# Performance work log

Hardware: AMD Instinct MI355X
Metric: run time of the kernel (lower is better)

Reference implementation:

```python
import jax, jax.numpy as jnp
import numpy as np

EMBED = 1024
HEADS = 16
HEAD_DIM = EMBED // HEADS


def setup_inputs() -> dict:
    key = jax.random.key(0)
    k_x, k_q, k_k, k_v, k_o, k_b = jax.random.split(key, 6)
    s = 1.0 / np.sqrt(EMBED)
    return {
        "x": jax.random.normal(k_x, (4, 2048, EMBED), dtype=jnp.float32),
        "Wq": jax.random.uniform(k_q, (EMBED, EMBED), jnp.float32, -s, s),
        "Wk": jax.random.uniform(k_k, (EMBED, EMBED), jnp.float32, -s, s),
        "Wv": jax.random.uniform(k_v, (EMBED, EMBED), jnp.float32, -s, s),
        "Wo": jax.random.uniform(k_o, (EMBED, EMBED), jnp.float32, -s, s),
        "bo": jax.random.uniform(k_b, (EMBED,), jnp.float32, -s, s),
    }


def reference(x, Wq, Wk, Wv, Wo, bo):
    B, S, E = x.shape
    H, D = HEADS, HEAD_DIM
    # torch nn.Linear: y = x @ W.T
    q = (x @ Wq.T).reshape(B, S, H, D).transpose(0, 2, 1, 3)  # [B,H,S,D]
    k = (x @ Wk.T).reshape(B, S, H, D).transpose(0, 2, 1, 3)
    v = (x @ Wv.T).reshape(B, S, H, D).transpose(0, 2, 1, 3)
    # NOTE: module scales by sqrt(embed_size), not sqrt(head_dim)
    scores = jnp.einsum("bhqd,bhkd->bhqk", q, k) / jnp.sqrt(jnp.float32(E))
    causal = jnp.triu(jnp.ones((S, S), dtype=bool), k=1)
    scores = jnp.where(causal, -jnp.inf, scores)
    attn = jax.nn.softmax(scores, axis=-1)
    out = jnp.einsum("bhqk,bhkd->bhqd", attn, v)  # [B,H,S,D]
    out = out.transpose(0, 2, 1, 3).reshape(B, S, E)
    return out @ Wo.T + bo
```

## Files before the change

### kernel.cpp

```cpp
#include <hip/hip_runtime.h>


#define E_DIM 1024
#define S_LEN 2048
#define BATCH 4
#define NHEAD 16
#define HDIM  64

using short8 = __attribute__((ext_vector_type(8))) short;
using f32x4  = __attribute__((ext_vector_type(4))) float;
using f32x16 = __attribute__((ext_vector_type(16))) float;
using i32x4  = __attribute__((ext_vector_type(4))) int;

#define GLD16(gp, lp) __builtin_amdgcn_global_load_lds( \
    (const __attribute__((address_space(1))) void*)(gp), \
    (__attribute__((address_space(3))) void*)(lp), 16, 0, 0)

__device__ inline unsigned short f2bf(float f) {
    unsigned int u = __builtin_bit_cast(unsigned int, f);
    u += 0x7FFFu + ((u >> 16) & 1u);
    return (unsigned short)(u >> 16);
}

__device__ inline unsigned int cvt_pk_bf16(float a, float b) {
    unsigned int r;
    asm("v_cvt_pk_bf16_f32 %0, %1, %2" : "=v"(r) : "v"(a), "v"(b));
    return r;
}

__global__ __launch_bounds__(256) void cvt_all(
        const float* __restrict__ x,  const float* __restrict__ wq,
        const float* __restrict__ wk, const float* __restrict__ wv,
        const float* __restrict__ wo,
        unsigned short* __restrict__ xb, unsigned short* __restrict__ wb) {
    const int bid = blockIdx.x;
    const float* src;
    unsigned short* dst;
    int blk;
    if (bid < 8192) { src = x; dst = xb; blk = bid; }
    else {
        const int wsel = (bid - 8192) >> 10;
        blk = (bid - 8192) & 1023;
        src = (wsel == 0) ? wq : (wsel == 1) ? wk : (wsel == 2) ? wv : wo;
        dst = wb + (size_t)wsel * 1048576;
    }
    const int i = (blk * 256 + threadIdx.x) * 4;
    float4 v = *reinterpret_cast<const float4*>(src + i);
    ushort4 o;
    o.x = f2bf(v.x); o.y = f2bf(v.y); o.z = f2bf(v.z); o.w = f2bf(v.w);
    *reinterpret_cast<ushort4*>(dst + i) = o;
}

__global__ __launch_bounds__(256) void gemm_qkv(
        const unsigned short* __restrict__ xb,
        const unsigned short* __restrict__ wb,
        unsigned short* __restrict__ qkv) {
    const int z = blockIdx.z;
    const unsigned short* Bw = wb + (size_t)z * (E_DIM * E_DIM);
    unsigned short* Out = qkv + (size_t)z * ((size_t)BATCH * NHEAD * S_LEN * HDIM);
    const int m0 = blockIdx.x * 128, n0 = blockIdx.y * 128;
    const int tid = threadIdx.x;
    const int lane = tid & 63, w = tid >> 6;
    const int wm = w >> 1, wn = w & 1;
    const int col = lane & 15, hi = lane >> 4;

    __shared__ __align__(16) unsigned short Alds[128 * 32];
    __shared__ __align__(16) unsigned short Blds[128 * 32];

    const int srow = tid >> 2;
    const int sc8  = (tid & 3) * 8;
    const int wofs = w * 512;

    f32x4 acc[4][4] = {};

    for (int kt = 0; kt < E_DIM / 32; ++kt) {
        const int k0 = kt * 32;
        GLD16(xb + (size_t)(m0 + srow) * E_DIM + k0 + sc8,       &Alds[wofs]);
        GLD16(xb + (size_t)(m0 + 64 + srow) * E_DIM + k0 + sc8,  &Alds[2048 + wofs]);
        GLD16(Bw + (size_t)(n0 + srow) * E_DIM + k0 + sc8,       &Blds[wofs]);
        GLD16(Bw + (size_t)(n0 + 64 + srow) * E_DIM + k0 + sc8,  &Blds[2048 + wofs]);
        __syncthreads();
        short8 af[4], bf[4];
#pragma unroll
        for (int mt = 0; mt < 4; ++mt)
            af[mt] = *reinterpret_cast<const short8*>(&Alds[(wm * 64 + mt * 16 + col) * 32 + hi * 8]);
#pragma unroll
        for (int nt = 0; nt < 4; ++nt)
            bf[nt] = *reinterpret_cast<const short8*>(&Blds[(wn * 64 + nt * 16 + col) * 32 + hi * 8]);
#pragma unroll
        for (int mt = 0; mt < 4; ++mt)
#pragma unroll
            for (int nt = 0; nt < 4; ++nt)
                acc[mt][nt] = __builtin_amdgcn_mfma_f32_16x16x32_bf16(af[mt], bf[nt], acc[mt][nt], 0, 0, 0);
        __syncthreads();
    }

    const float scale = (z == 0) ? (0.03125f * 1.44269504f) : 1.0f;
#pragma unroll
    for (int mt = 0; mt < 4; ++mt) {
#pragma unroll
        for (int nt = 0; nt < 4; ++nt) {
#pragma unroll
            for (int b = 0; b < 4; ++b) {
                int m = m0 + wm * 64 + mt * 16 + hi * 4 + b;
                int n = n0 + wn * 64 + nt * 16 + col;
                int bidx = m >> 11, s = m & 2047;
                int h = n >> 6, d = n & 63;
                size_t off = (((size_t)(bidx * NHEAD + h)) * S_LEN + s) * HDIM + d;
                Out[off] = f2bf(acc[mt][nt][b] * scale);
            }
        }
    }
}

__global__ __launch_bounds__(256, 4) void attn_fwd(
        const unsigned short* __restrict__ Q,
        const unsigned short* __restrict__ K,
        const unsigned short* __restrict__ V,
        unsigned short* __restrict__ Out) {
    const int g = blockIdx.x;
    const int qt = 15 - (g >> 6);
    const int bh = (g & 7) + ((g >> 3) & 7) * 8;
    const int b_idx = bh >> 4, h = bh & 15;
    const int tid = threadIdx.x, lane = tid & 63, w = tid >> 6;
    const int l31 = lane & 31, b5 = lane >> 5;
    const bool lo32 = (b5 == 0);
    const int rsw = (l31 & 7) << 3;

    const unsigned short* Qb = Q + (size_t)bh * (S_LEN * HDIM);
    const unsigned short* Kb = K + (size_t)bh * (S_LEN * HDIM);
    const unsigned short* Vb = V + (size_t)bh * (S_LEN * HDIM);

    __shared__ __align__(16) unsigned short Klds[64 * 64];
    __shared__ __align__(16) unsigned short Vt[64 * 64];

    const int kr = tid >> 3, kc8 = (tid & 7) * 8;
    const int ksw = kc8 ^ ((kr & 7) << 3);
    const int vr = tid & 63, vc8 = (tid >> 6) * 8;

    const int nt = 2 * qt + 2;
    const int q0w = qt * 128 + w * 32;
    const int qg = q0w + l31;

    short8 qf[4];
    {
        const unsigned short* qrow = Qb + (size_t)qg * HDIM;
#pragma unroll
        for (int dc = 0; dc < 4; ++dc)
            qf[dc] = *reinterpret_cast<const short8*>(qrow + dc * 16 + b5 * 8);
    }

    f32x16 ot0 = {}, ot1 = {};
    float mrun = -INFINITY, lsum = 0.f;

    short8 pk0 = *reinterpret_cast<const short8*>(Kb + (size_t)kr * HDIM + kc8);
    short8 pk1 = *reinterpret_cast<const short8*>(Kb + (size_t)(32 + kr) * HDIM + kc8);
    short8 pv0 = *reinterpret_cast<const short8*>(Vb + (size_t)vr * HDIM + vc8);
    short8 pv1 = *reinterpret_cast<const short8*>(Vb + (size_t)vr * HDIM + vc8 + 32);

    for (int t = 0; t < nt; ++t) {
        const int kv0 = t * 64;
        __syncthreads();
        *reinterpret_cast<short8*>(&Klds[kr * 64 + ksw]) = pk0;
        *reinterpret_cast<short8*>(&Klds[(kr + 32) * 64 + ksw]) = pk1;
#pragma unroll
        for (int j = 0; j < 8; ++j) {
            const int d0 = vc8 + j;
            const int vsw = vr ^ ((d0 & 7) << 3);
            Vt[d0 * 64 + vsw]        = (unsigned short)pv0[j];
            Vt[(d0 + 32) * 64 + vsw] = (unsigned short)pv1[j];
        }
        if (t < nt - 1) {
            const int kn = kv0 + 64;
            pk0 = *reinterpret_cast<const short8*>(Kb + (size_t)(kn + kr) * HDIM + kc8);
            pk1 = *reinterpret_cast<const short8*>(Kb + (size_t)(kn + 32 + kr) * HDIM + kc8);
            pv0 = *reinterpret_cast<const short8*>(Vb + (size_t)(kn + vr) * HDIM + vc8);
            pv1 = *reinterpret_cast<const short8*>(Vb + (size_t)(kn + vr) * HDIM + vc8 + 32);
        }
        __syncthreads();

        if (kv0 <= q0w + 31) {
            f32x16 st0 = {}, st1 = {};
            __builtin_amdgcn_s_setprio(1);
#pragma unroll
            for (int dc = 0; dc < 4; ++dc) {
                const int co = dc * 16 + b5 * 8;
                short8 kfA = *reinterpret_cast<const short8*>(&Klds[l31 * 64 + (co ^ rsw)]);
                short8 kfB = *reinterpret_cast<const short8*>(&Klds[(32 + l31) * 64 + (co ^ rsw)]);
                st0 = __builtin_amdgcn_mfma_f32_32x32x16_bf16(kfA, qf[dc], st0, 0, 0, 0);
                st1 = __builtin_amdgcn_mfma_f32_32x32x16_bf16(kfB, qf[dc], st1, 0, 0, 0);
            }
            __builtin_amdgcn_s_setprio(0);

            if (kv0 + 63 > q0w) {
#pragma unroll
                for (int r = 0; r < 16; ++r) {
                    const int krow = (r & 3) + 8 * (r >> 2) + 4 * b5;
                    if (kv0 + krow > qg)      st0[r] = -INFINITY;
                    if (kv0 + 32 + krow > qg) st1[r] = -INFINITY;
                }
            }

            float vm = st0[0];
#pragma unroll
            for (int r = 1; r < 16; ++r) vm = fmaxf(vm, st0[r]);
#pragma unroll
            for (int r = 0; r < 16; ++r) vm = fmaxf(vm, st1[r]);
            vm = fmaxf(vm, __shfl_xor(vm, 32));
            if (__any(vm > mrun + 11.5f)) {
                const float mnew = fmaxf(mrun, vm);
                const float fac = exp2f(mrun - mnew);
                mrun = mnew;
                lsum *= fac;
#pragma unroll
                for (int r = 0; r < 16; ++r) { ot0[r] *= fac; ot1[r] *= fac; }
            }

#pragma unroll
            for (int kc = 0; kc < 4; ++kc) {
                const int r0 = (kc & 1) * 8;
                float pe[8];
#pragma unroll
                for (int i = 0; i < 8; ++i) {
                    const float sv = (kc < 2) ? st0[r0 + i] : st1[r0 + i];
                    pe[i] = exp2f(sv - mrun);
                    lsum += pe[i];
                }
                const unsigned int W0 = cvt_pk_bf16(pe[0], pe[1]);
                const unsigned int W1 = cvt_pk_bf16(pe[2], pe[3]);
                const unsigned int W2 = cvt_pk_bf16(pe[4], pe[5]);
                const unsigned int W3 = cvt_pk_bf16(pe[6], pe[7]);
                const unsigned int t0 = (unsigned int)__shfl_xor((int)W0, 32);
                const unsigned int t1 = (unsigned int)__shfl_xor((int)W1, 32);
                const unsigned int t2 = (unsigned int)__shfl_xor((int)W2, 32);
                const unsigned int t3 = (unsigned int)__shfl_xor((int)W3, 32);
                i32x4 wv;
                wv[0] = (int)(lo32 ? W0 : t2);
                wv[1] = (int)(lo32 ? W1 : t3);
                wv[2] = (int)(lo32 ? t0 : W2);
                wv[3] = (int)(lo32 ? t1 : W3);
                const short8 pf = __builtin_bit_cast(short8, wv);

                const int co = kc * 16 + b5 * 8;
                short8 vf0 = *reinterpret_cast<const short8*>(&Vt[l31 * 64 + (co ^ rsw)]);
                short8 vf1 = *reinterpret_cast<const short8*>(&Vt[(32 + l31) * 64 + (co ^ rsw)]);
                __builtin_amdgcn_s_setprio(1);
                ot0 = __builtin_amdgcn_mfma_f32_32x32x16_bf16(vf0, pf, ot0, 0, 0, 0);
                ot1 = __builtin_amdgcn_mfma_f32_32x32x16_bf16(vf1, pf, ot1, 0, 0, 0);
                __builtin_amdgcn_s_setprio(0);
            }
        }
    }

    const float lfull = lsum + __shfl_xor(lsum, 32);
    const float inv = 1.0f / lfull;
    const size_t base = ((size_t)(b_idx * S_LEN + qg)) * E_DIM + h * HDIM;
#pragma unroll
    for (int r2 = 0; r2 < 8; ++r2) {
        const int d0 = 2 * (r2 & 1) + 8 * (r2 >> 1) + 4 * b5;
        const unsigned int u0 = cvt_pk_bf16(ot0[2 * r2] * inv, ot0[2 * r2 + 1] * inv);
        const unsigned int u1 = cvt_pk_bf16(ot1[2 * r2] * inv, ot1[2 * r2 + 1] * inv);
        *reinterpret_cast<unsigned int*>(const_cast<unsigned short*>(Out) + base + d0) = u0;
        *reinterpret_cast<unsigned int*>(const_cast<unsigned short*>(Out) + base + 32 + d0) = u1;
    }
}

__global__ __launch_bounds__(256) void gemm_out(
        const unsigned short* __restrict__ Ab,
        const unsigned short* __restrict__ Bw,
        const float* __restrict__ bias,
        float* __restrict__ Out) {
    const int m0 = blockIdx.x * 128, n0 = blockIdx.y * 128;
    const int tid = threadIdx.x;
    const int lane = tid & 63, w = tid >> 6;
    const int wm = w >> 1, wn = w & 1;
    const int col = lane & 15, hi = lane >> 4;

    __shared__ __align__(16) unsigned short Alds[128 * 32];
    __shared__ __align__(16) unsigned short Blds[128 * 32];

    const int srow = tid >> 2;
    const int sc8  = (tid & 3) * 8;
    const int wofs = w * 512;

    f32x4 acc[4][4] = {};

    for (int kt = 0; kt < E_DIM / 32; ++kt) {
        const int k0 = kt * 32;
        GLD16(Ab + (size_t)(m0 + srow) * E_DIM + k0 + sc8,       &Alds[wofs]);
        GLD16(Ab + (size_t)(m0 + 64 + srow) * E_DIM + k0 + sc8,  &Alds[2048 + wofs]);
        GLD16(Bw + (size_t)(n0 + srow) * E_DIM + k0 + sc8,       &Blds[wofs]);
        GLD16(Bw + (size_t)(n0 + 64 + srow) * E_DIM + k0 + sc8,  &Blds[2048 + wofs]);
        __syncthreads();
        short8 af[4], bf[4];
#pragma unroll
        for (int mt = 0; mt < 4; ++mt)
            af[mt] = *reinterpret_cast<const short8*>(&Alds[(wm * 64 + mt * 16 + col) * 32 + hi * 8]);
#pragma unroll
        for (int nt = 0; nt < 4; ++nt)
            bf[nt] = *reinterpret_cast<const short8*>(&Blds[(wn * 64 + nt * 16 + col) * 32 + hi * 8]);
#pragma unroll
        for (int mt = 0; mt < 4; ++mt)
#pragma unroll
            for (int nt = 0; nt < 4; ++nt)
                acc[mt][nt] = __builtin_amdgcn_mfma_f32_16x16x32_bf16(af[mt], bf[nt], acc[mt][nt], 0, 0, 0);
        __syncthreads();
    }

#pragma unroll
    for (int mt = 0; mt < 4; ++mt) {
#pragma unroll
        for (int nt = 0; nt < 4; ++nt) {
#pragma unroll
            for (int b = 0; b < 4; ++b) {
                int m = m0 + wm * 64 + mt * 16 + hi * 4 + b;
                int n = n0 + wn * 64 + nt * 16 + col;
                Out[(size_t)m * E_DIM + n] = acc[mt][nt][b] + bias[n];
            }
        }
    }
}

extern "C" void kernel_launch(void* const* d_in, const int* in_sizes, int n_in,
                              void* d_out, int out_size, void* d_ws, size_t ws_size,
                              hipStream_t stream) {
    const float* x  = (const float*)d_in[0];
    const float* Wq = (const float*)d_in[1];
    const float* Wk = (const float*)d_in[2];
    const float* Wv = (const float*)d_in[3];
    const float* Wo = (const float*)d_in[4];
    const float* bo = (const float*)d_in[5];
    float* out = (float*)d_out;

    unsigned short* ws   = (unsigned short*)d_ws;
    unsigned short* xb   = ws;
    unsigned short* wb   = xb + (size_t)8192 * 1024;
    unsigned short* qkv  = wb + (size_t)4 * 1024 * 1024;
    unsigned short* attn = qkv + (size_t)3 * 8192 * 1024;

    cvt_all<<<12288, 256, 0, stream>>>(x, Wq, Wk, Wv, Wo, xb, wb);
    gemm_qkv<<<dim3(64, 8, 3), 256, 0, stream>>>(xb, wb, qkv);
    attn_fwd<<<1024, 256, 0, stream>>>(qkv, qkv + 8388608, qkv + 2 * 8388608, attn);
    gemm_out<<<dim3(64, 8), 256, 0, stream>>>(attn, wb + 3 * 1048576, bo, out);
}
```

Baseline: 196.2 us.

## Load K fragments directly into registers and double-buffer V in LDS

Drops the shared-memory K tile. Each wave now loads its K MFMA fragments straight from global memory into registers, prefetching the next tile right after the QK^T MFMAs. V gets a double-buffered LDS tile so one of the two per-iteration barriers can go, and the row-max reduction becomes a tree. This removes LDS write/read traffic and a barrier for K, at the cost of four times more global (L2) K reads per block and higher register pressure under the 256x4 launch bound.

Result: slower. 274.2 us (+39.7%).

```diff
diff --git a/kernel.cpp b/kernel.cpp
--- a/kernel.cpp
+++ b/kernel.cpp
@@ -131,11 +131,8 @@
     const unsigned short* Kb = K + (size_t)bh * (S_LEN * HDIM);
     const unsigned short* Vb = V + (size_t)bh * (S_LEN * HDIM);
 
-    __shared__ __align__(16) unsigned short Klds[64 * 64];
-    __shared__ __align__(16) unsigned short Vt[64 * 64];
-
-    const int kr = tid >> 3, kc8 = (tid & 7) * 8;
-    const int ksw = kc8 ^ ((kr & 7) << 3);
+    __shared__ __align__(16) unsigned short Vt[2][64 * 64];
+
     const int vr = tid & 63, vc8 = (tid >> 6) * 8;
 
     const int nt = 2 * qt + 2;
@@ -153,27 +150,30 @@
     f32x16 ot0 = {}, ot1 = {};
     float mrun = -INFINITY, lsum = 0.f;
 
-    short8 pk0 = *reinterpret_cast<const short8*>(Kb + (size_t)kr * HDIM + kc8);
-    short8 pk1 = *reinterpret_cast<const short8*>(Kb + (size_t)(32 + kr) * HDIM + kc8);
     short8 pv0 = *reinterpret_cast<const short8*>(Vb + (size_t)vr * HDIM + vc8);
     short8 pv1 = *reinterpret_cast<const short8*>(Vb + (size_t)vr * HDIM + vc8 + 32);
+    short8 kf0[4], kf1[4];
+    {
+        const size_t ro = (size_t)l31 * HDIM + b5 * 8;
+#pragma unroll
+        for (int dc = 0; dc < 4; ++dc) {
+            kf0[dc] = *reinterpret_cast<const short8*>(Kb + ro + dc * 16);
+            kf1[dc] = *reinterpret_cast<const short8*>(Kb + ro + 32 * HDIM + dc * 16);
+        }
+    }
 
     for (int t = 0; t < nt; ++t) {
         const int kv0 = t * 64;
-        __syncthreads();
-        *reinterpret_cast<short8*>(&Klds[kr * 64 + ksw]) = pk0;
-        *reinterpret_cast<short8*>(&Klds[(kr + 32) * 64 + ksw]) = pk1;
+        unsigned short* Vw = &Vt[t & 1][0];
 #pragma unroll
         for (int j = 0; j < 8; ++j) {
             const int d0 = vc8 + j;
             const int vsw = vr ^ ((d0 & 7) << 3);
-            Vt[d0 * 64 + vsw]        = (unsigned short)pv0[j];
-            Vt[(d0 + 32) * 64 + vsw] = (unsigned short)pv1[j];
+            Vw[d0 * 64 + vsw]        = (unsigned short)pv0[j];
+            Vw[(d0 + 32) * 64 + vsw] = (unsigned short)pv1[j];
         }
         if (t < nt - 1) {
             const int kn = kv0 + 64;
-            pk0 = *reinterpret_cast<const short8*>(Kb + (size_t)(kn + kr) * HDIM + kc8);
-            pk1 = *reinterpret_cast<const short8*>(Kb + (size_t)(kn + 32 + kr) * HDIM + kc8);
             pv0 = *reinterpret_cast<const short8*>(Vb + (size_t)(kn + vr) * HDIM + vc8);
             pv1 = *reinterpret_cast<const short8*>(Vb + (size_t)(kn + vr) * HDIM + vc8 + 32);
         }
@@ -184,13 +184,19 @@
             __builtin_amdgcn_s_setprio(1);
 #pragma unroll
             for (int dc = 0; dc < 4; ++dc) {
-                const int co = dc * 16 + b5 * 8;
-                short8 kfA = *reinterpret_cast<const short8*>(&Klds[l31 * 64 + (co ^ rsw)]);
-                short8 kfB = *reinterpret_cast<const short8*>(&Klds[(32 + l31) * 64 + (co ^ rsw)]);
-                st0 = __builtin_amdgcn_mfma_f32_32x32x16_bf16(kfA, qf[dc], st0, 0, 0, 0);
-                st1 = __builtin_amdgcn_mfma_f32_32x32x16_bf16(kfB, qf[dc], st1, 0, 0, 0);
+                st0 = __builtin_amdgcn_mfma_f32_32x32x16_bf16(kf0[dc], qf[dc], st0, 0, 0, 0);
+                st1 = __builtin_amdgcn_mfma_f32_32x32x16_bf16(kf1[dc], qf[dc], st1, 0, 0, 0);
             }
             __builtin_amdgcn_s_setprio(0);
+
+            if (t < nt - 1) {
+                const size_t ro = (size_t)(kv0 + 64 + l31) * HDIM + b5 * 8;
+#pragma unroll
+                for (int dc = 0; dc < 4; ++dc) {
+                    kf0[dc] = *reinterpret_cast<const short8*>(Kb + ro + dc * 16);
+                    kf1[dc] = *reinterpret_cast<const short8*>(Kb + ro + 32 * HDIM + dc * 16);
+                }
+            }
 
             if (kv0 + 63 > q0w) {
 #pragma unroll
@@ -201,11 +207,14 @@
                 }
             }
 
-            float vm = st0[0];
-#pragma unroll
-            for (int r = 1; r < 16; ++r) vm = fmaxf(vm, st0[r]);
-#pragma unroll
-            for (int r = 0; r < 16; ++r) vm = fmaxf(vm, st1[r]);
+            float tm[16];
+#pragma unroll
+            for (int r = 0; r < 16; ++r) tm[r] = fmaxf(st0[r], st1[r]);
+#pragma unroll
+            for (int r = 0; r < 8; ++r) tm[r] = fmaxf(tm[r], tm[r + 8]);
+#pragma unroll
+            for (int r = 0; r < 4; ++r) tm[r] = fmaxf(tm[r], tm[r + 4]);
+            float vm = fmaxf(fmaxf(tm[0], tm[1]), fmaxf(tm[2], tm[3]));
             vm = fmaxf(vm, __shfl_xor(vm, 32));
             if (__any(vm > mrun + 11.5f)) {
                 const float mnew = fmaxf(mrun, vm);
@@ -242,8 +251,9 @@
                 const short8 pf = __builtin_bit_cast(short8, wv);
 
                 const int co = kc * 16 + b5 * 8;
-                short8 vf0 = *reinterpret_cast<const short8*>(&Vt[l31 * 64 + (co ^ rsw)]);
-                short8 vf1 = *reinterpret_cast<const short8*>(&Vt[(32 + l31) * 64 + (co ^ rsw)]);
+                const unsigned short* Vc = &Vt[t & 1][0];
+                short8 vf0 = *reinterpret_cast<const short8*>(&Vc[l31 * 64 + (co ^ rsw)]);
+                short8 vf1 = *reinterpret_cast<const short8*>(&Vc[(32 + l31) * 64 + (co ^ rsw)]);
                 __builtin_amdgcn_s_setprio(1);
                 ot0 = __builtin_amdgcn_mfma_f32_32x32x16_bf16(vf0, pf, ot0, 0, 0, 0);
                 ot1 = __builtin_amdgcn_mfma_f32_32x32x16_bf16(vf1, pf, ot1, 0, 0, 0);
```

## Use 256-row query and key tiles with 512-thread blocks and async K loads

Applied to the files above, without the earlier changes.

The attention kernel now uses 512-thread blocks covering 256 query rows and stages 256 keys per iteration, with four 64-key sub-steps of compute per stage. K is copied straight into LDS with global_load_lds instead of passing through registers, and the row-max reduction becomes a tree. Larger tiles mean fewer barriers and more reuse of each K/V tile per block. The cost is four times the LDS per block, lower occupancy, coarser causal granularity that leaves more threads idle, and only 512 blocks in the grid.

Measured after the change: 178.3 us. 9.1% less time.

```diff
diff --git a/kernel.cpp b/kernel.cpp
--- a/kernel.cpp
+++ b/kernel.cpp
@@ -113,13 +113,13 @@
     }
 }
 
-__global__ __launch_bounds__(256, 4) void attn_fwd(
+__global__ __launch_bounds__(512, 2) void attn_fwd(
         const unsigned short* __restrict__ Q,
         const unsigned short* __restrict__ K,
         const unsigned short* __restrict__ V,
         unsigned short* __restrict__ Out) {
     const int g = blockIdx.x;
-    const int qt = 15 - (g >> 6);
+    const int qt = 7 - (g >> 6);
     const int bh = (g & 7) + ((g >> 3) & 7) * 8;
     const int b_idx = bh >> 4, h = bh & 15;
     const int tid = threadIdx.x, lane = tid & 63, w = tid >> 6;
@@ -131,15 +131,15 @@
     const unsigned short* Kb = K + (size_t)bh * (S_LEN * HDIM);
     const unsigned short* Vb = V + (size_t)bh * (S_LEN * HDIM);
 
-    __shared__ __align__(16) unsigned short Klds[64 * 64];
-    __shared__ __align__(16) unsigned short Vt[64 * 64];
-
-    const int kr = tid >> 3, kc8 = (tid & 7) * 8;
-    const int ksw = kc8 ^ ((kr & 7) << 3);
+    __shared__ __align__(16) unsigned short Klds[256 * 64];
+    __shared__ __align__(16) unsigned short Vt[64 * 256];
+
+    const int krl  = lane >> 3;
+    const int kcsw = ((lane & 7) * 8) ^ (krl << 3);
     const int vr = tid & 63, vc8 = (tid >> 6) * 8;
 
-    const int nt = 2 * qt + 2;
-    const int q0w = qt * 128 + w * 32;
+    const int nt = qt + 1;
+    const int q0w = qt * 256 + w * 32;
     const int qg = q0w + l31;
 
     short8 qf[4];
@@ -153,59 +153,80 @@
     f32x16 ot0 = {}, ot1 = {};
     float mrun = -INFINITY, lsum = 0.f;
 
-    short8 pk0 = *reinterpret_cast<const short8*>(Kb + (size_t)kr * HDIM + kc8);
-    short8 pk1 = *reinterpret_cast<const short8*>(Kb + (size_t)(32 + kr) * HDIM + kc8);
-    short8 pv0 = *reinterpret_cast<const short8*>(Vb + (size_t)vr * HDIM + vc8);
-    short8 pv1 = *reinterpret_cast<const short8*>(Vb + (size_t)vr * HDIM + vc8 + 32);
+    short8 pv0 = *reinterpret_cast<const short8*>(Vb + (size_t)(vr) * HDIM + vc8);
+    short8 pv1 = *reinterpret_cast<const short8*>(Vb + (size_t)(64 + vr) * HDIM + vc8);
+    short8 pv2 = *reinterpret_cast<const short8*>(Vb + (size_t)(128 + vr) * HDIM + vc8);
+    short8 pv3 = *reinterpret_cast<const short8*>(Vb + (size_t)(192 + vr) * HDIM + vc8);
 
     for (int t = 0; t < nt; ++t) {
-        const int kv0 = t * 64;
-        __syncthreads();
-        *reinterpret_cast<short8*>(&Klds[kr * 64 + ksw]) = pk0;
-        *reinterpret_cast<short8*>(&Klds[(kr + 32) * 64 + ksw]) = pk1;
+        const int kv0 = t * 256;
+        __syncthreads();
+#pragma unroll
+        for (int i = 0; i < 4; ++i) {
+            const int rowbase = 8 * (8 * i + w);
+            GLD16(Kb + (size_t)(kv0 + rowbase + krl) * HDIM + kcsw,
+                  &Klds[rowbase * 64]);
+        }
 #pragma unroll
         for (int j = 0; j < 8; ++j) {
             const int d0 = vc8 + j;
-            const int vsw = vr ^ ((d0 & 7) << 3);
-            Vt[d0 * 64 + vsw]        = (unsigned short)pv0[j];
-            Vt[(d0 + 32) * 64 + vsw] = (unsigned short)pv1[j];
+            const int sj = (d0 & 7) << 3;
+            Vt[d0 * 256 + ((vr)       ^ sj)] = (unsigned short)pv0[j];
+            Vt[d0 * 256 + ((64 + vr)  ^ sj)] = (unsigned short)pv1[j];
+            Vt[d0 * 256 + ((128 + vr) ^ sj)] = (unsigned short)pv2[j];
+            Vt[d0 * 256 + ((192 + vr) ^ sj)] = (unsigned short)pv3[j];
         }
         if (t < nt - 1) {
-            const int kn = kv0 + 64;
-            pk0 = *reinterpret_cast<const short8*>(Kb + (size_t)(kn + kr) * HDIM + kc8);
-            pk1 = *reinterpret_cast<const short8*>(Kb + (size_t)(kn + 32 + kr) * HDIM + kc8);
+            const int kn = kv0 + 256;
             pv0 = *reinterpret_cast<const short8*>(Vb + (size_t)(kn + vr) * HDIM + vc8);
-            pv1 = *reinterpret_cast<const short8*>(Vb + (size_t)(kn + vr) * HDIM + vc8 + 32);
-        }
-        __syncthreads();
-
-        if (kv0 <= q0w + 31) {
+            pv1 = *reinterpret_cast<const short8*>(Vb + (size_t)(kn + 64 + vr) * HDIM + vc8);
+            pv2 = *reinterpret_cast<const short8*>(Vb + (size_t)(kn + 128 + vr) * HDIM + vc8);
+            pv3 = *reinterpret_cast<const short8*>(Vb + (size_t)(kn + 192 + vr) * HDIM + vc8);
+        }
+        __syncthreads();
+
+#pragma unroll
+        for (int s4 = 0; s4 < 4; ++s4) {
+            const int kvs = kv0 + 64 * s4;
+            if (kvs > q0w + 31) break;
+            const int ksb = 64 * s4;
+
             f32x16 st0 = {}, st1 = {};
             __builtin_amdgcn_s_setprio(1);
 #pragma unroll
             for (int dc = 0; dc < 4; ++dc) {
                 const int co = dc * 16 + b5 * 8;
-                short8 kfA = *reinterpret_cast<const short8*>(&Klds[l31 * 64 + (co ^ rsw)]);
-                short8 kfB = *reinterpret_cast<const short8*>(&Klds[(32 + l31) * 64 + (co ^ rsw)]);
+                short8 kfA = *reinterpret_cast<const short8*>(&Klds[(ksb + l31) * 64 + (co ^ rsw)]);
+                short8 kfB = *reinterpret_cast<const short8*>(&Klds[(ksb + 32 + l31) * 64 + (co ^ rsw)]);
                 st0 = __builtin_amdgcn_mfma_f32_32x32x16_bf16(kfA, qf[dc], st0, 0, 0, 0);
                 st1 = __builtin_amdgcn_mfma_f32_32x32x16_bf16(kfB, qf[dc], st1, 0, 0, 0);
             }
             __builtin_amdgcn_s_setprio(0);
 
-            if (kv0 + 63 > q0w) {
+            if (kvs + 63 > q0w) {
 #pragma unroll
                 for (int r = 0; r < 16; ++r) {
                     const int krow = (r & 3) + 8 * (r >> 2) + 4 * b5;
-                    if (kv0 + krow > qg)      st0[r] = -INFINITY;
-                    if (kv0 + 32 + krow > qg) st1[r] = -INFINITY;
+                    if (kvs + krow > qg)      st0[r] = -INFINITY;
+                    if (kvs + 32 + krow > qg) st1[r] = -INFINITY;
                 }
             }
 
-            float vm = st0[0];
-#pragma unroll
-            for (int r = 1; r < 16; ++r) vm = fmaxf(vm, st0[r]);
-#pragma unroll
-            for (int r = 0; r < 16; ++r) vm = fmaxf(vm, st1[r]);
+            float tm0 = fmaxf(st0[0], st1[0]), tm1 = fmaxf(st0[1], st1[1]);
+            float tm2 = fmaxf(st0[2], st1[2]), tm3 = fmaxf(st0[3], st1[3]);
+            float tm4 = fmaxf(st0[4], st1[4]), tm5 = fmaxf(st0[5], st1[5]);
+            float tm6 = fmaxf(st0[6], st1[6]), tm7 = fmaxf(st0[7], st1[7]);
+            tm0 = fmaxf(tm0, fmaxf(st0[8],  st1[8]));
+            tm1 = fmaxf(tm1, fmaxf(st0[9],  st1[9]));
+            tm2 = fmaxf(tm2, fmaxf(st0[10], st1[10]));
+            tm3 = fmaxf(tm3, fmaxf(st0[11], st1[11]));
+            tm4 = fmaxf(tm4, fmaxf(st0[12], st1[12]));
+            tm5 = fmaxf(tm5, fmaxf(st0[13], st1[13]));
+            tm6 = fmaxf(tm6, fmaxf(st0[14], st1[14]));
+            tm7 = fmaxf(tm7, fmaxf(st0[15], st1[15]));
+            tm0 = fmaxf(tm0, tm4); tm1 = fmaxf(tm1, tm5);
+            tm2 = fmaxf(tm2, tm6); tm3 = fmaxf(tm3, tm7);
+            float vm = fmaxf(fmaxf(tm0, tm1), fmaxf(tm2, tm3));
             vm = fmaxf(vm, __shfl_xor(vm, 32));
             if (__any(vm > mrun + 11.5f)) {
                 const float mnew = fmaxf(mrun, vm);
@@ -241,9 +262,9 @@
                 wv[3] = (int)(lo32 ? t1 : W3);
                 const short8 pf = __builtin_bit_cast(short8, wv);
 
-                const int co = kc * 16 + b5 * 8;
-                short8 vf0 = *reinterpret_cast<const short8*>(&Vt[l31 * 64 + (co ^ rsw)]);
-                short8 vf1 = *reinterpret_cast<const short8*>(&Vt[(32 + l31) * 64 + (co ^ rsw)]);
+                const int ck = ksb + kc * 16 + b5 * 8;
+                short8 vf0 = *reinterpret_cast<const short8*>(&Vt[l31 * 256 + (ck ^ rsw)]);
+                short8 vf1 = *reinterpret_cast<const short8*>(&Vt[(32 + l31) * 256 + (ck ^ rsw)]);
                 __builtin_amdgcn_s_setprio(1);
                 ot0 = __builtin_amdgcn_mfma_f32_32x32x16_bf16(vf0, pf, ot0, 0, 0, 0);
                 ot1 = __builtin_amdgcn_mfma_f32_32x32x16_bf16(vf1, pf, ot1, 0, 0, 0);
@@ -340,6 +361,6 @@
 
     cvt_all<<<12288, 256, 0, stream>>>(x, Wq, Wk, Wv, Wo, xb, wb);
     gemm_qkv<<<dim3(64, 8, 3), 256, 0, stream>>>(xb, wb, qkv);
-    attn_fwd<<<1024, 256, 0, stream>>>(qkv, qkv + 8388608, qkv + 2 * 8388608, attn);
+    attn_fwd<<<512, 512, 0, stream>>>(qkv, qkv + 8388608, qkv + 2 * 8388608, attn);
     gemm_out<<<dim3(64, 8), 256, 0, stream>>>(attn, wb + 3 * 1048576, bo, out);
 }
```
